# Optimization experiments

Hardware: AMD Instinct MI355X
Metric: run time of the kernel (lower is better)

Reference implementation:

```python
import jax, jax.numpy as jnp
import numpy as np

N = 131072      # number of query points
NB = 24         # SMPL bones
H = 128         # MLP hidden width
MAX_STEPS = 10
CVG_THRESH = 1e-5
DVG_THRESH = 1.0
EPS = 1e-6


def setup_inputs() -> dict:
    key = jax.random.key(0)
    k = jax.random.split(key, 8)
    xd = 0.5 * jax.random.normal(k[0], (N, 3), jnp.float32)          # deformed-space targets
    x_init = (xd + 0.05 * jax.random.normal(k[1], (N, 3), jnp.float32))[..., None]  # [N,3,1]
    J_inv_init = jnp.broadcast_to(jnp.eye(3, dtype=jnp.float32), (N, 3, 3)) \
        + 0.01 * jax.random.normal(k[2], (N, 3, 3), jnp.float32)
    # bone transforms near identity so the iteration stays below dvg_thresh
    R = jnp.broadcast_to(jnp.eye(3, dtype=jnp.float32), (NB, 3, 3)) \
        + 0.01 * jax.random.normal(k[3], (NB, 3, 3), jnp.float32)
    t = 0.02 * jax.random.normal(k[4], (NB, 3, 1), jnp.float32)
    tfs = jnp.concatenate([R, t], axis=-1)  # [NB,3,4]
    W0 = jax.random.normal(k[5], (3, H), jnp.float32) / jnp.sqrt(3.0)
    b0 = jnp.zeros((H,), jnp.float32)
    W1 = jax.random.normal(k[6], (H, H), jnp.float32) / jnp.sqrt(float(H))
    b1 = jnp.zeros((H,), jnp.float32)
    W2 = jax.random.normal(k[7], (H, NB), jnp.float32) / jnp.sqrt(float(H))
    b2 = jnp.zeros((NB,), jnp.float32)
    return {"xd": xd, "x_init": x_init, "J_inv_init": J_inv_init, "tfs": tfs,
            "W0": W0, "b0": b0, "W1": W1, "b1": b1, "W2": W2, "b2": b2}


def _broyden(xd, x_init, J_inv_init, tfs, W0, b0, W1, b1, W2, b2):
    def g(x):
        # skinning-weight MLP + LBS blend: g(x) = LBS(x) - xd, shape [N,3,1]
        xs = x[..., 0]                                    # [N,3]
        h = jax.nn.softplus(xs @ W0 + b0)
        h = jax.nn.softplus(h @ W1 + b1)
        w = jax.nn.softmax(h @ W2 + b2, axis=-1)          # [N,NB]
        T = jnp.einsum('nj,jab->nab', w, tfs)             # [N,3,4] blended transform
        pred = jnp.einsum('nab,nb->na', T[:, :, :3], xs) + T[:, :, 3]
        return (pred - xd)[..., None]

    x = x_init
    Jinv = J_inv_init
    gx = g(x)
    update = -jnp.einsum('nab,nbk->nak', Jinv, gx)
    gn_opt = jnp.linalg.norm(gx[..., 0], axis=-1)         # [N]
    x_opt = x
    ids = jnp.ones((x.shape[0],), bool)

    def step(carry, _):
        x, gx, Jinv, update, x_opt, gn_opt, ids = carry
        m = ids[:, None, None]
        dx = jnp.where(m, update, 0.0)                    # masked delta_x
        x = x + dx
        dgx = jnp.where(m, g(x) - gx, 0.0)                # masked delta_gx
        gx = gx + dgx
        gn = jnp.linalg.norm(gx[..., 0], axis=-1)
        better = gn < gn_opt
        gn_opt = jnp.where(better, gn, gn_opt)
        x_opt = jnp.where(better[:, None, None], x, x_opt)
        ids = (gn_opt > CVG_THRESH) & (gn < DVG_THRESH)
        # Broyden (good) rank-1 inverse-Jacobian update, per point
        vT = jnp.einsum('nak,nab->nkb', dx, Jinv)         # dx^T J_inv  [N,1,3]
        a = dx - jnp.einsum('nab,nbk->nak', Jinv, dgx)    # [N,3,1]
        b = jnp.einsum('nkb,nbj->nkj', vT, dgx)           # [N,1,1]
        b = b + jnp.where(b >= 0, EPS, -EPS)
        u = a / b
        Jinv = Jinv + jnp.where(ids[:, None, None], jnp.einsum('nak,nkb->nab', u, vT), 0.0)
        update = -jnp.einsum('nab,nbk->nak', Jinv, gx)
        return (x, gx, Jinv, update, x_opt, gn_opt, ids), None

    carry, _ = jax.lax.scan(step, (x, gx, Jinv, update, x_opt, gn_opt, ids),
                            None, length=MAX_STEPS)
    x_opt, gn_opt = carry[4], carry[5]
    return x_opt, gn_opt, gn_opt < CVG_THRESH


def reference(xd, x_init, J_inv_init, tfs, W0, b0, W1, b1, W2, b2):
    res, diff, valid = _broyden(xd, x_init, J_inv_init, tfs, W0, b0, W1, b1, W2, b2)
    # the torch broyden detaches the iterate / best-norm buffers
    return jax.lax.stop_gradient(res), jax.lax.stop_gradient(diff), valid
```

## Files before the change

kernel.cpp:

```cpp
#include <hip/hip_runtime.h>
#include <math.h>

#define NBLEND 24
#define HDIM 128
#define KQ 32
#define MAX_STEPS 10
#define CVG_T 1e-5f
#define DVG_T 1.0f
#define EPS_B 1e-6f

typedef float v2f __attribute__((ext_vector_type(2)));

#if __has_builtin(__builtin_elementwise_fma)
#define VFMA(a, b, c) __builtin_elementwise_fma((a), (b), (c))
#else
static __device__ __forceinline__ v2f VFMA(v2f a, v2f b, v2f c) {
    v2f r; r.x = fmaf(a.x, b.x, c.x); r.y = fmaf(a.y, b.y, c.y); return r;
}
#endif

__device__ __forceinline__ float softplus_f(float x) {
    float e = __expf(-fabsf(x));
    return fmaxf(x, 0.0f) + __logf(1.0f + e);
}

__device__ __forceinline__ void eval_g_quad(
    float* __restrict__ hbuf,
    int w, int lane,
    const float* __restrict__ W0, const float* __restrict__ b0,
    const float* __restrict__ W1, const float* __restrict__ b1,
    const float* __restrict__ W2, const float* __restrict__ b2,
    const float* __restrict__ tfs,
    float x0, float x1, float x2,
    float xd0, float xd1, float xd2,
    float& g0, float& g1, float& g2)
{
    v2f* part = (v2f*)hbuf;
    v2f vx0 = {x0, x0}, vx1 = {x1, x1}, vx2 = {x2, x2};

    {
        const int jb = w * KQ;
        #pragma unroll 4
        for (int jj = 0; jj < KQ; jj += 2) {
            const int j = jb + jj;
            v2f z = *(const v2f*)(b0 + j);
            z = VFMA(vx0, *(const v2f*)(W0 + j), z);
            z = VFMA(vx1, *(const v2f*)(W0 + HDIM + j), z);
            z = VFMA(vx2, *(const v2f*)(W0 + 2 * HDIM + j), z);
            hbuf[j * 64 + lane]       = softplus_f(z.x);
            hbuf[(j + 1) * 64 + lane] = softplus_f(z.y);
        }
    }
    __syncthreads();

    v2f acc[KQ / 2];
    {
        const v2f* __restrict__ b1v = (const v2f*)(b1 + w * KQ);
        #pragma unroll
        for (int kk = 0; kk < KQ / 2; ++kk) acc[kk] = b1v[kk];
    }
    const float* __restrict__ W1h = W1 + w * KQ;
    #pragma unroll 2
    for (int j = 0; j < HDIM; j += 2) {
        float ha = hbuf[j * 64 + lane];
        float hb = hbuf[(j + 1) * 64 + lane];
        const v2f* __restrict__ r0 = (const v2f*)(W1h + j * HDIM);
        const v2f* __restrict__ r1 = (const v2f*)(W1h + (j + 1) * HDIM);
        v2f hva = {ha, ha}, hvb = {hb, hb};
        #pragma unroll
        for (int kk = 0; kk < KQ / 2; ++kk) acc[kk] = VFMA(hva, r0[kk], acc[kk]);
        #pragma unroll
        for (int kk = 0; kk < KQ / 2; ++kk) acc[kk] = VFMA(hvb, r1[kk], acc[kk]);
    }
    #pragma unroll
    for (int kk = 0; kk < KQ / 2; ++kk) {
        acc[kk].x = softplus_f(acc[kk].x);
        acc[kk].y = softplus_f(acc[kk].y);
    }

    v2f lgp[NBLEND / 2];
    #pragma unroll
    for (int m2 = 0; m2 < NBLEND / 2; ++m2) lgp[m2] = (v2f){0.f, 0.f};
    const float* __restrict__ W2h = W2 + w * KQ * NBLEND;
    #pragma unroll
    for (int kk = 0; kk < KQ; ++kk) {
        float h1 = (kk & 1) ? acc[kk >> 1].y : acc[kk >> 1].x;
        v2f hv = {h1, h1};
        const v2f* __restrict__ w2r = (const v2f*)(W2h + kk * NBLEND);
        #pragma unroll
        for (int m2 = 0; m2 < NBLEND / 2; ++m2) lgp[m2] = VFMA(hv, w2r[m2], lgp[m2]);
    }

    __syncthreads();
    #pragma unroll
    for (int m2 = 0; m2 < NBLEND / 2; ++m2) part[(w * 12 + m2) * 64 + lane] = lgp[m2];
    __syncthreads();
    v2f lg[NBLEND / 2];
    {
        const v2f* __restrict__ b2v = (const v2f*)b2;
        #pragma unroll
        for (int m2 = 0; m2 < NBLEND / 2; ++m2)
            lg[m2] = ((b2v[m2] + part[(0 * 12 + m2) * 64 + lane])
                      + part[(1 * 12 + m2) * 64 + lane])
                     + (part[(2 * 12 + m2) * 64 + lane]
                        + part[(3 * 12 + m2) * 64 + lane]);
    }
    __syncthreads();

    float M = -3.0e38f;
    #pragma unroll
    for (int m2 = 0; m2 < NBLEND / 2; ++m2)
        M = fmaxf(M, fmaxf(lg[m2].x, lg[m2].y));

    float S = 0.f;
    v2f T[6];
    #pragma unroll
    for (int t = 0; t < 6; ++t) T[t] = (v2f){0.f, 0.f};
    #pragma unroll
    for (int m = 0; m < NBLEND; ++m) {
        float lgm = (m & 1) ? lg[m >> 1].y : lg[m >> 1].x;
        float e = __expf(lgm - M);
        S += e;
        const v2f* __restrict__ tf = (const v2f*)(tfs + m * 12);
        v2f ev = {e, e};
        #pragma unroll
        for (int t = 0; t < 6; ++t) T[t] = VFMA(ev, tf[t], T[t]);
    }
    float inv = 1.0f / S;
    g0 = inv * fmaf(T[0].x, x0, fmaf(T[0].y, x1, fmaf(T[1].x, x2, T[1].y))) - xd0;
    g1 = inv * fmaf(T[2].x, x0, fmaf(T[2].y, x1, fmaf(T[3].x, x2, T[3].y))) - xd1;
    g2 = inv * fmaf(T[4].x, x0, fmaf(T[4].y, x1, fmaf(T[5].x, x2, T[5].y))) - xd2;
}

__global__ void __launch_bounds__(256)
broyden_quad_kernel(const float* __restrict__ xd_p,
                    const float* __restrict__ x_init,
                    const float* __restrict__ Jinv_init,
                    const float* __restrict__ tfs,
                    const float* __restrict__ W0, const float* __restrict__ b0,
                    const float* __restrict__ W1, const float* __restrict__ b1,
                    const float* __restrict__ W2, const float* __restrict__ b2,
                    float* __restrict__ out, int N)
{
    __shared__ __align__(16) float hbuf[HDIM * 64];
    const int tid = threadIdx.x;
    const int lane = tid & 63;
    const int w = __builtin_amdgcn_readfirstlane(tid >> 6);
    const int n = blockIdx.x * 64 + lane;

    float xd0 = xd_p[n * 3 + 0], xd1 = xd_p[n * 3 + 1], xd2 = xd_p[n * 3 + 2];
    float x0 = x_init[n * 3 + 0], x1 = x_init[n * 3 + 1], x2 = x_init[n * 3 + 2];
    float J0 = Jinv_init[n * 9 + 0], J1 = Jinv_init[n * 9 + 1], J2 = Jinv_init[n * 9 + 2];
    float J3 = Jinv_init[n * 9 + 3], J4 = Jinv_init[n * 9 + 4], J5 = Jinv_init[n * 9 + 5];
    float J6 = Jinv_init[n * 9 + 6], J7 = Jinv_init[n * 9 + 7], J8 = Jinv_init[n * 9 + 8];

    float g0, g1, g2;
    eval_g_quad(hbuf, w, lane, W0, b0, W1, b1, W2, b2, tfs,
                x0, x1, x2, xd0, xd1, xd2, g0, g1, g2);

    float u0 = -(fmaf(J0, g0, fmaf(J1, g1, J2 * g2)));
    float u1 = -(fmaf(J3, g0, fmaf(J4, g1, J5 * g2)));
    float u2 = -(fmaf(J6, g0, fmaf(J7, g1, J8 * g2)));

    float gn_opt = sqrtf(g0 * g0 + g1 * g1 + g2 * g2);
    float xo0 = x0, xo1 = x1, xo2 = x2;
    bool ids = true;

    for (int step = 0; step < MAX_STEPS; ++step) {
        if (__ballot(ids) == 0ull) break;

        float dx0 = ids ? u0 : 0.f, dx1 = ids ? u1 : 0.f, dx2 = ids ? u2 : 0.f;
        x0 += dx0; x1 += dx1; x2 += dx2;

        float ng0, ng1, ng2;
        eval_g_quad(hbuf, w, lane, W0, b0, W1, b1, W2, b2, tfs,
                    x0, x1, x2, xd0, xd1, xd2, ng0, ng1, ng2);
        float dg0 = ng0 - g0, dg1 = ng1 - g1, dg2 = ng2 - g2;
        g0 = ng0; g1 = ng1; g2 = ng2;

        float gn = sqrtf(g0 * g0 + g1 * g1 + g2 * g2);
        bool better = gn < gn_opt;
        if (better) { gn_opt = gn; xo0 = x0; xo1 = x1; xo2 = x2; }
        bool ids_new = (gn_opt > CVG_T) && (gn < DVG_T);

        float vT0 = fmaf(dx0, J0, fmaf(dx1, J3, dx2 * J6));
        float vT1 = fmaf(dx0, J1, fmaf(dx1, J4, dx2 * J7));
        float vT2 = fmaf(dx0, J2, fmaf(dx1, J5, dx2 * J8));
        float a0 = dx0 - fmaf(J0, dg0, fmaf(J1, dg1, J2 * dg2));
        float a1 = dx1 - fmaf(J3, dg0, fmaf(J4, dg1, J5 * dg2));
        float a2 = dx2 - fmaf(J6, dg0, fmaf(J7, dg1, J8 * dg2));
        float bb = fmaf(vT0, dg0, fmaf(vT1, dg1, vT2 * dg2));
        bb += (bb >= 0.f) ? EPS_B : -EPS_B;
        float iu0 = ids_new ? (a0 / bb) : 0.f;
        float iu1 = ids_new ? (a1 / bb) : 0.f;
        float iu2 = ids_new ? (a2 / bb) : 0.f;
        J0 = fmaf(iu0, vT0, J0); J1 = fmaf(iu0, vT1, J1); J2 = fmaf(iu0, vT2, J2);
        J3 = fmaf(iu1, vT0, J3); J4 = fmaf(iu1, vT1, J4); J5 = fmaf(iu1, vT2, J5);
        J6 = fmaf(iu2, vT0, J6); J7 = fmaf(iu2, vT1, J7); J8 = fmaf(iu2, vT2, J8);

        u0 = -(fmaf(J0, g0, fmaf(J1, g1, J2 * g2)));
        u1 = -(fmaf(J3, g0, fmaf(J4, g1, J5 * g2)));
        u2 = -(fmaf(J6, g0, fmaf(J7, g1, J8 * g2)));
        ids = ids_new;
    }

    if (w == 0) {
        out[n * 3 + 0] = xo0;
        out[n * 3 + 1] = xo1;
        out[n * 3 + 2] = xo2;
        out[3 * N + n] = gn_opt;
        out[4 * N + n] = (gn_opt < CVG_T) ? 1.0f : 0.0f;
    }
}

extern "C" void kernel_launch(void* const* d_in, const int* in_sizes, int n_in,
                              void* d_out, int out_size, void* d_ws, size_t ws_size,
                              hipStream_t stream) {
    const float* xd     = (const float*)d_in[0];
    const float* x_init = (const float*)d_in[1];
    const float* Jinv   = (const float*)d_in[2];
    const float* tfs    = (const float*)d_in[3];
    const float* W0     = (const float*)d_in[4];
    const float* b0     = (const float*)d_in[5];
    const float* W1     = (const float*)d_in[6];
    const float* b1     = (const float*)d_in[7];
    const float* W2     = (const float*)d_in[8];
    const float* b2     = (const float*)d_in[9];
    float* out = (float*)d_out;

    const int N = in_sizes[0] / 3;
    dim3 block(256);
    dim3 grid((N + 63) / 64);

    hipLaunchKernelGGL(broyden_quad_kernel, grid, block, 0, stream,
                       xd, x_init, Jinv, tfs, W0, b0, W1, b1, W2, b2, out, N);
}
```

Baseline: 311.1 us.

## Use persistent blocks with atomic work-stealing over point chunks

Replaces the one-block-per-64-points grid with a persistent grid of at most 1280 blocks. Each block repeatedly claims a chunk index through a global atomic counter in the workspace, which is zeroed with a memset before launch. The goal is to cut block launch and tail imbalance across the 2048 chunks. It also raises the unroll of the hidden-layer loop from 2 to 4. The cost is extra syncthreads per chunk, an atomic per chunk, a memset launch, and possible register-pressure changes from the larger unroll.

Result: slower. 489.1 us (+57.2%).

```diff
diff --git a/kernel.cpp b/kernel.cpp
--- a/kernel.cpp
+++ b/kernel.cpp
@@ -60,7 +60,7 @@
         for (int kk = 0; kk < KQ / 2; ++kk) acc[kk] = b1v[kk];
     }
     const float* __restrict__ W1h = W1 + w * KQ;
-    #pragma unroll 2
+    #pragma unroll 4
     for (int j = 0; j < HDIM; j += 2) {
         float ha = hbuf[j * 64 + lane];
         float hb = hbuf[(j + 1) * 64 + lane];
@@ -132,22 +132,15 @@
     g2 = inv * fmaf(T[4].x, x0, fmaf(T[4].y, x1, fmaf(T[5].x, x2, T[5].y))) - xd2;
 }
 
-__global__ void __launch_bounds__(256)
-broyden_quad_kernel(const float* __restrict__ xd_p,
-                    const float* __restrict__ x_init,
-                    const float* __restrict__ Jinv_init,
-                    const float* __restrict__ tfs,
-                    const float* __restrict__ W0, const float* __restrict__ b0,
-                    const float* __restrict__ W1, const float* __restrict__ b1,
-                    const float* __restrict__ W2, const float* __restrict__ b2,
-                    float* __restrict__ out, int N)
-{
-    __shared__ __align__(16) float hbuf[HDIM * 64];
-    const int tid = threadIdx.x;
-    const int lane = tid & 63;
-    const int w = __builtin_amdgcn_readfirstlane(tid >> 6);
-    const int n = blockIdx.x * 64 + lane;
-
+__device__ __forceinline__ void solve_chunk(
+    float* __restrict__ hbuf, int w, int lane, int n, int N,
+    const float* __restrict__ xd_p, const float* __restrict__ x_init,
+    const float* __restrict__ Jinv_init, const float* __restrict__ tfs,
+    const float* __restrict__ W0, const float* __restrict__ b0,
+    const float* __restrict__ W1, const float* __restrict__ b1,
+    const float* __restrict__ W2, const float* __restrict__ b2,
+    float* __restrict__ out)
+{
     float xd0 = xd_p[n * 3 + 0], xd1 = xd_p[n * 3 + 1], xd2 = xd_p[n * 3 + 2];
     float x0 = x_init[n * 3 + 0], x1 = x_init[n * 3 + 1], x2 = x_init[n * 3 + 2];
     float J0 = Jinv_init[n * 9 + 0], J1 = Jinv_init[n * 9 + 1], J2 = Jinv_init[n * 9 + 2];
@@ -213,6 +206,54 @@
     }
 }
 
+__global__ void __launch_bounds__(256)
+broyden_persist_kernel(const float* __restrict__ xd_p,
+                       const float* __restrict__ x_init,
+                       const float* __restrict__ Jinv_init,
+                       const float* __restrict__ tfs,
+                       const float* __restrict__ W0, const float* __restrict__ b0,
+                       const float* __restrict__ W1, const float* __restrict__ b1,
+                       const float* __restrict__ W2, const float* __restrict__ b2,
+                       float* __restrict__ out, int* __restrict__ ctr,
+                       int nchunks, int N)
+{
+    __shared__ __align__(16) float hbuf[HDIM * 64];
+    const int tid = threadIdx.x;
+    const int lane = tid & 63;
+    const int w = __builtin_amdgcn_readfirstlane(tid >> 6);
+
+    for (;;) {
+        if (tid == 0) ((int*)hbuf)[0] = atomicAdd(ctr, 1);
+        __syncthreads();
+        const int chunk = ((int*)hbuf)[0];
+        __syncthreads();
+        if (chunk >= nchunks) break;
+
+        const int n = chunk * 64 + lane;
+        solve_chunk(hbuf, w, lane, n, N, xd_p, x_init, Jinv_init, tfs,
+                    W0, b0, W1, b1, W2, b2, out);
+    }
+}
+
+__global__ void __launch_bounds__(256)
+broyden_quad_kernel(const float* __restrict__ xd_p,
+                    const float* __restrict__ x_init,
+                    const float* __restrict__ Jinv_init,
+                    const float* __restrict__ tfs,
+                    const float* __restrict__ W0, const float* __restrict__ b0,
+                    const float* __restrict__ W1, const float* __restrict__ b1,
+                    const float* __restrict__ W2, const float* __restrict__ b2,
+                    float* __restrict__ out, int N)
+{
+    __shared__ __align__(16) float hbuf[HDIM * 64];
+    const int tid = threadIdx.x;
+    const int lane = tid & 63;
+    const int w = __builtin_amdgcn_readfirstlane(tid >> 6);
+    const int n = blockIdx.x * 64 + lane;
+    solve_chunk(hbuf, w, lane, n, N, xd_p, x_init, Jinv_init, tfs,
+                W0, b0, W1, b1, W2, b2, out);
+}
+
 extern "C" void kernel_launch(void* const* d_in, const int* in_sizes, int n_in,
                               void* d_out, int out_size, void* d_ws, size_t ws_size,
                               hipStream_t stream) {
@@ -229,9 +270,17 @@
     float* out = (float*)d_out;
 
     const int N = in_sizes[0] / 3;
-    dim3 block(256);
-    dim3 grid((N + 63) / 64);
-
-    hipLaunchKernelGGL(broyden_quad_kernel, grid, block, 0, stream,
-                       xd, x_init, Jinv, tfs, W0, b0, W1, b1, W2, b2, out, N);
-}
+    const int nchunks = (N + 63) / 64;
+
+    if (ws_size >= 16) {
+        int* ctr = (int*)d_ws;
+        hipMemsetAsync(ctr, 0, 16, stream);
+        const int nblk = (nchunks < 1280) ? nchunks : 1280;
+        hipLaunchKernelGGL(broyden_persist_kernel, dim3(nblk), dim3(256), 0, stream,
+                           xd, x_init, Jinv, tfs, W0, b0, W1, b1, W2, b2,
+                           out, ctr, nchunks, N);
+    } else {
+        hipLaunchKernelGGL(broyden_quad_kernel, dim3(nchunks), dim3(256), 0, stream,
+                           xd, x_init, Jinv, tfs, W0, b0, W1, b1, W2, b2, out, N);
+    }
+}
```
